# Performance work log

Measured on AMD Instinct MI355X. Metric: run time of the kernel, lower is better.

Reference implementation:

```python
import jax, jax.numpy as jnp
import numpy as np

B, S, D, H, HID = 2, 2048, 512, 8, 2048
DH = D // H
EPS = 1e-5


def _ln(x, g, b):
    mu = jnp.mean(x, axis=-1, keepdims=True)
    var = jnp.mean(jnp.square(x - mu), axis=-1, keepdims=True)
    return (x - mu) * jax.lax.rsqrt(var + EPS) * g + b


def setup_inputs() -> dict:
    key = jax.random.key(0)
    ks = jax.random.split(key, 12)
    s = 0.02
    return {
        "x": jax.random.normal(ks[0], (B, S, D), jnp.float32),
        "prev": jax.random.normal(ks[1], (B, H, S, S), jnp.float32),
        # weights stored as [in, out]
        "kqv_w": jax.random.normal(ks[2], (D, 3 * D), jnp.float32) * s,
        "kqv_b": jnp.zeros((3 * D,), jnp.float32),
        "out_w": jax.random.normal(ks[3], (D, D), jnp.float32) * s,
        "out_b": jnp.zeros((D,), jnp.float32),
        "fc1_w": jax.random.normal(ks[4], (D, HID), jnp.float32) * s,
        "fc1_b": jnp.zeros((HID,), jnp.float32),
        "fc2_w": jax.random.normal(ks[5], (HID, D), jnp.float32) * s,
        "fc2_b": jnp.zeros((D,), jnp.float32),
        "ln1_g": jnp.ones((D,), jnp.float32),
        "ln1_b": jnp.zeros((D,), jnp.float32),
        "ln2_g": jnp.ones((D,), jnp.float32),
        "ln2_b": jnp.zeros((D,), jnp.float32),
    }


def reference(x, prev, kqv_w, kqv_b, out_w, out_b, fc1_w, fc1_b, fc2_w, fc2_b,
              ln1_g, ln1_b, ln2_g, ln2_b):
    scale = 1.0 / np.sqrt(DH)
    kqv = x @ kqv_w + kqv_b                      # [B,S,3D]
    # torch.chunk order: key, query, value
    k, q, v = jnp.split(kqv, 3, axis=-1)
    k = k.reshape(B, S, H, DH)
    q = q.reshape(B, S, H, DH)
    v = v.reshape(B, S, H, DH)
    energy = scale * jnp.einsum('bqhd,bkhd->bhqk', q, k) + prev  # [B,H,S,S]
    attn = jax.nn.softmax(energy, axis=-1)
    ctx = jnp.einsum('bhqk,bkhd->bqhd', attn, v).reshape(B, S, D)
    attn_out = ctx @ out_w + out_b
    h = _ln(attn_out + x, ln1_g, ln1_b)          # post-norm 1
    ff = jax.nn.gelu(h @ fc1_w + fc1_b, approximate=False) @ fc2_w + fc2_b
    out = _ln(ff + h, ln2_g, ln2_b)              # post-norm 2
    return (out, energy)
```

## Files before the change

kernel.cpp:

```cpp
#include <hip/hip_runtime.h>
#include <math.h>

#define S_ 2048
#define D_ 512
#define H_ 8
#define DH_ 64
#define HID_ 2048
#define NT_ 4096
#define K3D_ 1536

typedef unsigned short u16;
typedef __bf16 bf16x8 __attribute__((ext_vector_type(8)));
typedef float f32x4 __attribute__((ext_vector_type(4)));

__device__ __forceinline__ float b2f(u16 u) {
  union { unsigned int i; float f; } v; v.i = ((unsigned int)u) << 16; return v.f;
}
__device__ __forceinline__ u16 f2b(float f) {
  union { float f; unsigned int i; } v; v.f = f;
  unsigned int u = v.i;
  u += 0x7fffu + ((u >> 16) & 1u);
  return (u16)(u >> 16);
}

__global__ __launch_bounds__(256) void cvt_kernel(
    const float* __restrict__ in, u16* __restrict__ out, int n8) {
  int i = blockIdx.x * 256 + threadIdx.x;
  if (i >= n8) return;
  size_t base = (size_t)i * 8;
  float4 a = *(const float4*)(in + base);
  float4 b = *(const float4*)(in + base + 4);
  u16 ov[8] = {f2b(a.x), f2b(a.y), f2b(a.z), f2b(a.w),
               f2b(b.x), f2b(b.y), f2b(b.z), f2b(b.w)};
  *(uint4*)(out + base) = *(uint4*)ov;
}

__global__ __launch_bounds__(256) void transpose_kernel(
    const float* __restrict__ in, u16* __restrict__ out, int R, int C) {
  int idx = blockIdx.x * 256 + threadIdx.x;
  if (idx >= R * C) return;
  int r = idx / C, c = idx % C;
  out[(size_t)c * R + r] = f2b(in[idx]);
}

__global__ __launch_bounds__(256) void vt_kernel(
    const u16* __restrict__ kqv, u16* __restrict__ vt) {
  int bh = blockIdx.y, b = bh >> 3, h = bh & 7;
  const u16* V = kqv + (size_t)b * S_ * K3D_ + 2 * D_ + h * DH_;
  u16* O = vt + (size_t)bh * DH_ * S_;
  int idx = blockIdx.x * 256 + threadIdx.x;
  int r = idx >> 6, c = idx & 63;
  O[(size_t)c * S_ + r] = V[(size_t)r * K3D_ + c];
}

__global__ __launch_bounds__(256) void gemm_bt(
    const u16* __restrict__ A, const u16* __restrict__ Bt,
    const float* __restrict__ bias, void* __restrict__ Cv,
    int K, int lda, int ldb, int ldc, int mode) {
  u16* Cb = (u16*)Cv;
  int tile_m = blockIdx.y * 64, tile_n = blockIdx.x * 64;

  __shared__ alignas(16) u16 As[64 * 40];
  __shared__ alignas(16) u16 Bs[64 * 40];

  int t = threadIdx.x;
  int w = t >> 6, lane = t & 63, quad = lane >> 4, l16 = lane & 15;
  int srow = t >> 2, schunk = (t & 3) * 8;

  f32x4 acc[4];
#pragma unroll
  for (int i = 0; i < 4; ++i) acc[i] = (f32x4){0.f, 0.f, 0.f, 0.f};

  for (int kb = 0; kb < K; kb += 32) {
    uint4 av = *(const uint4*)(A  + (size_t)(tile_m + srow) * lda + kb + schunk);
    uint4 bv = *(const uint4*)(Bt + (size_t)(tile_n + srow) * ldb + kb + schunk);
    __syncthreads();
    *(uint4*)(&As[srow * 40 + schunk]) = av;
    *(uint4*)(&Bs[srow * 40 + schunk]) = bv;
    __syncthreads();
    bf16x8 a = *(const bf16x8*)(&As[(w * 16 + l16) * 40 + quad * 8]);
#pragma unroll
    for (int nt = 0; nt < 4; ++nt) {
      bf16x8 b = *(const bf16x8*)(&Bs[(nt * 16 + l16) * 40 + quad * 8]);
      acc[nt] = __builtin_amdgcn_mfma_f32_16x16x32_bf16(a, b, acc[nt], 0, 0, 0);
    }
  }

#pragma unroll
  for (int nt = 0; nt < 4; ++nt) {
    int col = tile_n + nt * 16 + l16;
    float bcol = bias[col];
#pragma unroll
    for (int r = 0; r < 4; ++r) {
      int row = tile_m + w * 16 + quad * 4 + r;
      float v = acc[nt][r] + bcol;
      if (mode == 1) v = 0.5f * v * (1.f + erff(v * 0.70710678118654752f));
      Cb[(size_t)row * ldc + col] = f2b(v);
    }
  }
}

__global__ __launch_bounds__(256) void fused_attn(
    const u16* __restrict__ kqv, const u16* __restrict__ vt,
    const float* __restrict__ prev, float* __restrict__ energy,
    u16* __restrict__ ctx) {
  int bh = blockIdx.y, b = bh >> 3, h = bh & 7;
  int qbase = blockIdx.x * 64;

  const u16* Qp  = kqv + (size_t)b * S_ * K3D_ + D_ + h * DH_;
  const u16* Kp  = kqv + (size_t)b * S_ * K3D_ + h * DH_;
  const u16* Vtp = vt + (size_t)bh * DH_ * S_;
  const float* Pvp = prev + (size_t)bh * S_ * S_;
  float* Ep = energy + (size_t)bh * S_ * S_;

  int t = threadIdx.x;
  int w = t >> 6, lane = t & 63, quad = lane >> 4, l16 = lane & 15;

  __shared__ alignas(16) u16 KsB[2][64 * 72];
  __shared__ alignas(16) u16 VsB[2][64 * 72];
  __shared__ alignas(16) float Es[4][16 * 68];
  __shared__ alignas(16) u16 Pt[4][16 * 72];
  __shared__ float m_s[4][16];
  __shared__ float l_s[4][16];
  __shared__ float r_s[4][16];

  bf16x8 qf0, qf1;
  {
    const u16* qrow = Qp + (size_t)(qbase + w * 16 + l16) * K3D_;
    qf0 = *(const bf16x8*)(qrow + quad * 8);
    qf1 = *(const bf16x8*)(qrow + 32 + quad * 8);
  }

  if (lane < 16) { m_s[w][lane] = -1e30f; l_s[w][lane] = 0.f; }

  f32x4 oa[4];
#pragma unroll
  for (int i = 0; i < 4; ++i) oa[i] = (f32x4){0.f, 0.f, 0.f, 0.f};

  int c0 = t * 2, c1 = c0 + 1;
  int kr0 = c0 >> 3, ko0 = (c0 & 7) * 8;
  int kr1 = c1 >> 3, ko1 = (c1 & 7) * 8;

  {
    uint4 ka0 = *(const uint4*)(Kp + (size_t)kr0 * K3D_ + ko0);
    uint4 ka1 = *(const uint4*)(Kp + (size_t)kr1 * K3D_ + ko1);
    uint4 va0 = *(const uint4*)(Vtp + (size_t)kr0 * S_ + ko0);
    uint4 va1 = *(const uint4*)(Vtp + (size_t)kr1 * S_ + ko1);
    *(uint4*)(&KsB[0][kr0 * 72 + ko0]) = ka0;
    *(uint4*)(&KsB[0][kr1 * 72 + ko1]) = ka1;
    *(uint4*)(&VsB[0][kr0 * 72 + ko0]) = va0;
    *(uint4*)(&VsB[0][kr1 * 72 + ko1]) = va1;
  }
  __syncthreads();

  for (int it = 0; it < 32; ++it) {
    int cur = it & 1;
    int kb = it * 64;

    uint4 ka0, ka1, va0, va1;
    if (it < 31) {
      int kn = kb + 64;
      ka0 = *(const uint4*)(Kp + (size_t)(kn + kr0) * K3D_ + ko0);
      ka1 = *(const uint4*)(Kp + (size_t)(kn + kr1) * K3D_ + ko1);
      va0 = *(const uint4*)(Vtp + (size_t)kr0 * S_ + kn + ko0);
      va1 = *(const uint4*)(Vtp + (size_t)kr1 * S_ + kn + ko1);
    }

    const u16* Ks = KsB[cur];
    const u16* Vs = VsB[cur];

    f32x4 sa[4];
#pragma unroll
    for (int i = 0; i < 4; ++i) sa[i] = (f32x4){0.f, 0.f, 0.f, 0.f};
#pragma unroll
    for (int kc = 0; kc < 2; ++kc) {
      bf16x8 a = kc ? qf1 : qf0;
#pragma unroll
      for (int nt = 0; nt < 4; ++nt) {
        bf16x8 bk = *(const bf16x8*)(&Ks[(nt * 16 + l16) * 72 + kc * 32 + quad * 8]);
        sa[nt] = __builtin_amdgcn_mfma_f32_16x16x32_bf16(a, bk, sa[nt], 0, 0, 0);
      }
    }

#pragma unroll
    for (int nt = 0; nt < 4; ++nt)
#pragma unroll
      for (int r = 0; r < 4; ++r)
        Es[w][(quad * 4 + r) * 68 + nt * 16 + l16] = sa[nt][r] * 0.125f;
    asm volatile("" ::: "memory");

    float4 ek[4];
    float mt[4];
#pragma unroll
    for (int r4 = 0; r4 < 4; ++r4) {
      int row = r4 * 4 + quad;
      float4 e4 = *(const float4*)(&Es[w][row * 68 + l16 * 4]);
      size_t goff = (size_t)(qbase + w * 16 + row) * S_ + kb + l16 * 4;
      float4 p4 = *(const float4*)(Pvp + goff);
      e4.x += p4.x; e4.y += p4.y; e4.z += p4.z; e4.w += p4.w;
      *(float4*)(Ep + goff) = e4;
      ek[r4] = e4;
      mt[r4] = fmaxf(fmaxf(e4.x, e4.y), fmaxf(e4.z, e4.w));
    }
#pragma unroll
    for (int r4 = 0; r4 < 4; ++r4)
#pragma unroll
      for (int off = 1; off < 16; off <<= 1)
        mt[r4] = fmaxf(mt[r4], __shfl_xor(mt[r4], off, 16));
    if (l16 == 0) {
#pragma unroll
      for (int r4 = 0; r4 < 4; ++r4) {
        int row = r4 * 4 + quad;
        float mo = m_s[w][row];
        float mn = fmaxf(mo, mt[r4]);
        r_s[w][row] = __expf(mo - mn);
        m_s[w][row] = mn;
      }
    }
    asm volatile("" ::: "memory");

    float ls[4];
#pragma unroll
    for (int r4 = 0; r4 < 4; ++r4) {
      int row = r4 * 4 + quad;
      float mrow = m_s[w][row];
      float4 e4 = ek[r4];
      float p0 = __expf(e4.x - mrow), p1 = __expf(e4.y - mrow);
      float p2 = __expf(e4.z - mrow), p3 = __expf(e4.w - mrow);
      ls[r4] = (p0 + p1) + (p2 + p3);
      u16 pb[4] = {f2b(p0), f2b(p1), f2b(p2), f2b(p3)};
      *(uint2*)(&Pt[w][row * 72 + l16 * 4]) = *(uint2*)pb;
    }
#pragma unroll
    for (int r4 = 0; r4 < 4; ++r4)
#pragma unroll
      for (int off = 1; off < 16; off <<= 1)
        ls[r4] += __shfl_xor(ls[r4], off, 16);
    if (l16 == 0) {
#pragma unroll
      for (int r4 = 0; r4 < 4; ++r4) {
        int row = r4 * 4 + quad;
        l_s[w][row] = l_s[w][row] * r_s[w][row] + ls[r4];
      }
    }
#pragma unroll
    for (int rr = 0; rr < 4; ++rr) {
      float rf = r_s[w][quad * 4 + rr];
#pragma unroll
      for (int nt = 0; nt < 4; ++nt) oa[nt][rr] *= rf;
    }
    asm volatile("" ::: "memory");

#pragma unroll
    for (int kc = 0; kc < 2; ++kc) {
      bf16x8 a = *(const bf16x8*)(&Pt[w][l16 * 72 + kc * 32 + quad * 8]);
#pragma unroll
      for (int nt = 0; nt < 4; ++nt) {
        bf16x8 bv = *(const bf16x8*)(&Vs[(nt * 16 + l16) * 72 + kc * 32 + quad * 8]);
        oa[nt] = __builtin_amdgcn_mfma_f32_16x16x32_bf16(a, bv, oa[nt], 0, 0, 0);
      }
    }

    if (it < 31) {
      int nxt = cur ^ 1;
      *(uint4*)(&KsB[nxt][kr0 * 72 + ko0]) = ka0;
      *(uint4*)(&KsB[nxt][kr1 * 72 + ko1]) = ka1;
      *(uint4*)(&VsB[nxt][kr0 * 72 + ko0]) = va0;
      *(uint4*)(&VsB[nxt][kr1 * 72 + ko1]) = va1;
      __syncthreads();
    }
  }

  asm volatile("" ::: "memory");
  float il[4];
#pragma unroll
  for (int rr = 0; rr < 4; ++rr) il[rr] = 1.f / l_s[w][quad * 4 + rr];
#pragma unroll
  for (int nt = 0; nt < 4; ++nt) {
    int col = h * DH_ + nt * 16 + l16;
#pragma unroll
    for (int rr = 0; rr < 4; ++rr) {
      size_t row = (size_t)b * S_ + qbase + w * 16 + quad * 4 + rr;
      ctx[row * D_ + col] = f2b(oa[nt][rr] * il[rr]);
    }
  }
}

__global__ __launch_bounds__(256) void ln_kernel(
    const u16* __restrict__ a, const void* __restrict__ rsrc,
    const float* __restrict__ g, const float* __restrict__ be,
    void* __restrict__ o, int r_f32, int o_f32) {
  int row = blockIdx.x * 4 + (threadIdx.x >> 6);
  int lane = threadIdx.x & 63;
  size_t base = (size_t)row * D_ + lane * 8;
  uint4 av = *(const uint4*)(a + base);
  const u16* ap = (const u16*)&av;
  float rv[8];
  if (r_f32) {
    float4 r0 = *(const float4*)((const float*)rsrc + base);
    float4 r1 = *(const float4*)((const float*)rsrc + base + 4);
    rv[0] = r0.x; rv[1] = r0.y; rv[2] = r0.z; rv[3] = r0.w;
    rv[4] = r1.x; rv[5] = r1.y; rv[6] = r1.z; rv[7] = r1.w;
  } else {
    uint4 rr = *(const uint4*)((const u16*)rsrc + base);
    const u16* rp = (const u16*)&rr;
#pragma unroll
    for (int j = 0; j < 8; ++j) rv[j] = b2f(rp[j]);
  }
  float tv[8], s = 0.f, sq = 0.f;
#pragma unroll
  for (int j = 0; j < 8; ++j) {
    float xx = b2f(ap[j]) + rv[j];
    tv[j] = xx; s += xx; sq += xx * xx;
  }
#pragma unroll
  for (int off = 32; off; off >>= 1) {
    s  += __shfl_xor(s, off);
    sq += __shfl_xor(sq, off);
  }
  float mu  = s * (1.f / 512.f);
  float var = fmaxf(sq * (1.f / 512.f) - mu * mu, 0.f);
  float wv  = rsqrtf(var + 1e-5f);
  float4 g0 = *(const float4*)(g + lane * 8);
  float4 g1 = *(const float4*)(g + lane * 8 + 4);
  float4 b0 = *(const float4*)(be + lane * 8);
  float4 b1 = *(const float4*)(be + lane * 8 + 4);
  float gv[8] = {g0.x, g0.y, g0.z, g0.w, g1.x, g1.y, g1.z, g1.w};
  float bv[8] = {b0.x, b0.y, b0.z, b0.w, b1.x, b1.y, b1.z, b1.w};
  if (o_f32) {
    float ov[8];
#pragma unroll
    for (int j = 0; j < 8; ++j) ov[j] = (tv[j] - mu) * wv * gv[j] + bv[j];
    *(float4*)((float*)o + base)     = *(float4*)(ov);
    *(float4*)((float*)o + base + 4) = *(float4*)(ov + 4);
  } else {
    u16 ov[8];
#pragma unroll
    for (int j = 0; j < 8; ++j) ov[j] = f2b((tv[j] - mu) * wv * gv[j] + bv[j]);
    *(uint4*)((u16*)o + base) = *(uint4*)ov;
  }
}

extern "C" void kernel_launch(void* const* d_in, const int* in_sizes, int n_in,
                              void* d_out, int out_size, void* d_ws, size_t ws_size,
                              hipStream_t stream) {
  const float* x     = (const float*)d_in[0];
  const float* prev  = (const float*)d_in[1];
  const float* kqv_w = (const float*)d_in[2];
  const float* kqv_b = (const float*)d_in[3];
  const float* out_w = (const float*)d_in[4];
  const float* out_b = (const float*)d_in[5];
  const float* fc1_w = (const float*)d_in[6];
  const float* fc1_b = (const float*)d_in[7];
  const float* fc2_w = (const float*)d_in[8];
  const float* fc2_b = (const float*)d_in[9];
  const float* ln1_g = (const float*)d_in[10];
  const float* ln1_b = (const float*)d_in[11];
  const float* ln2_g = (const float*)d_in[12];
  const float* ln2_b = (const float*)d_in[13];

  float* outp   = (float*)d_out;
  float* energy = outp + (size_t)NT_ * D_;

  u16* ws = (u16*)d_ws;
  u16* R0 = ws;
  u16* R2 = R0 + (size_t)8388608;
  u16* R3 = R2 + (size_t)2097152;
  u16* R4 = R3 + (size_t)2097152;
  u16* WA = R4 + (size_t)2097152;

  u16* kqv    = R0;
  u16* vt     = R0 + (size_t)6291456;
  u16* attn   = R0;
  u16* ff     = R0;
  u16* ctx    = R2;  u16* f2     = R2;
  u16* hbuf   = R3;
  u16* xb     = R4;
  u16* fc1_wt = R4;  u16* fc2_wt = R4 + (size_t)1048576;
  u16* kqv_wt = WA;  u16* out_wt = WA;

  cvt_kernel<<<(NT_ * D_ / 8 + 255) / 256, 256, 0, stream>>>(x, xb, NT_ * D_ / 8);
  transpose_kernel<<<(D_ * K3D_ + 255) / 256, 256, 0, stream>>>(kqv_w, kqv_wt, D_, K3D_);

  gemm_bt<<<dim3(K3D_ / 64, NT_ / 64, 1), 256, 0, stream>>>(
      xb, kqv_wt, kqv_b, kqv, D_, D_, D_, K3D_, 0);

  transpose_kernel<<<(D_ * HID_ + 255) / 256, 256, 0, stream>>>(fc1_w, fc1_wt, D_, HID_);
  transpose_kernel<<<(HID_ * D_ + 255) / 256, 256, 0, stream>>>(fc2_w, fc2_wt, HID_, D_);
  transpose_kernel<<<(D_ * D_ + 255) / 256, 256, 0, stream>>>(out_w, out_wt, D_, D_);

  vt_kernel<<<dim3((S_ * DH_) / 256, 16), 256, 0, stream>>>(kqv, vt);

  fused_attn<<<dim3(S_ / 64, 16), 256, 0, stream>>>(kqv, vt, prev, energy, ctx);

  gemm_bt<<<dim3(D_ / 64, NT_ / 64, 1), 256, 0, stream>>>(
      ctx, out_wt, out_b, attn, D_, D_, D_, D_, 0);

  ln_kernel<<<NT_ / 4, 256, 0, stream>>>(attn, x, ln1_g, ln1_b, hbuf, 1, 0);

  gemm_bt<<<dim3(HID_ / 64, NT_ / 64, 1), 256, 0, stream>>>(
      hbuf, fc1_wt, fc1_b, ff, D_, D_, D_, HID_, 1);

  gemm_bt<<<dim3(D_ / 64, NT_ / 64, 1), 256, 0, stream>>>(
      ff, fc2_wt, fc2_b, f2, HID_, HID_, HID_, D_, 0);

  ln_kernel<<<NT_ / 4, 256, 0, stream>>>(f2, hbuf, ln2_g, ln2_b, outp, 0, 1);
}
```

Before: 661.3 us.

## Replace GEMM with larger-tile kernel using direct global-to-LDS loads

Replaces the 64x64 GEMM with a templated kernel using 128xBN tiles, a 2x2 wave layout and multiple MFMAs per K step for more register reuse. Tiles are loaded with global_load_lds straight into shared memory, skipping the trip through registers. The LDS padding is removed, which may add bank conflicts, and larger tiles mean fewer blocks for the narrow N=512 GEMMs.

After: 678.7 us. 1.03x slower.

```diff
diff --git a/kernel.cpp b/kernel.cpp
--- a/kernel.cpp
+++ b/kernel.cpp
@@ -12,6 +12,9 @@
 typedef unsigned short u16;
 typedef __bf16 bf16x8 __attribute__((ext_vector_type(8)));
 typedef float f32x4 __attribute__((ext_vector_type(4)));
+
+typedef const __attribute__((address_space(1))) unsigned int* gas_p;
+typedef __attribute__((address_space(3))) unsigned int* las_p;
 
 __device__ __forceinline__ float b2f(u16 u) {
   union { unsigned int i; float f; } v; v.i = ((unsigned int)u) << 16; return v.f;
@@ -53,49 +56,77 @@
   O[(size_t)c * S_ + r] = V[(size_t)r * K3D_ + c];
 }
 
-__global__ __launch_bounds__(256) void gemm_bt(
+template<int BN>
+__global__ __launch_bounds__(256) void gemm_glds(
     const u16* __restrict__ A, const u16* __restrict__ Bt,
-    const float* __restrict__ bias, void* __restrict__ Cv,
-    int K, int lda, int ldb, int ldc, int mode) {
-  u16* Cb = (u16*)Cv;
-  int tile_m = blockIdx.y * 64, tile_n = blockIdx.x * 64;
-
-  __shared__ alignas(16) u16 As[64 * 40];
-  __shared__ alignas(16) u16 Bs[64 * 40];
+    const float* __restrict__ bias, u16* __restrict__ C,
+    int K, int lda, int ldb, int ldc, int gelu) {
+  constexpr int BM = 128;
+  constexpr int NF = BN / 32;
+  constexpr int A_LOADS = BM / 64;
+  constexpr int B_LOADS = BN / 64;
+
+  __shared__ alignas(16) u16 As[BM * 32];
+  __shared__ alignas(16) u16 Bs[BN * 32];
 
   int t = threadIdx.x;
   int w = t >> 6, lane = t & 63, quad = lane >> 4, l16 = lane & 15;
-  int srow = t >> 2, schunk = (t & 3) * 8;
-
-  f32x4 acc[4];
-#pragma unroll
-  for (int i = 0; i < 4; ++i) acc[i] = (f32x4){0.f, 0.f, 0.f, 0.f};
+  int wr = w >> 1, wc = w & 1;
+  int tile_m = blockIdx.y * BM, tile_n = blockIdx.x * BN;
+
+  int srow = lane >> 2, schunk = (lane & 3) * 8;
+
+  f32x4 acc[4][NF];
+#pragma unroll
+  for (int i = 0; i < 4; ++i)
+#pragma unroll
+    for (int n = 0; n < NF; ++n) acc[i][n] = (f32x4){0.f, 0.f, 0.f, 0.f};
 
   for (int kb = 0; kb < K; kb += 32) {
-    uint4 av = *(const uint4*)(A  + (size_t)(tile_m + srow) * lda + kb + schunk);
-    uint4 bv = *(const uint4*)(Bt + (size_t)(tile_n + srow) * ldb + kb + schunk);
     __syncthreads();
-    *(uint4*)(&As[srow * 40 + schunk]) = av;
-    *(uint4*)(&Bs[srow * 40 + schunk]) = bv;
+#pragma unroll
+    for (int j = 0; j < A_LOADS; ++j) {
+      int jj = w * A_LOADS + j;
+      const u16* g = A + (size_t)(tile_m + jj * 16 + srow) * lda + kb + schunk;
+      __builtin_amdgcn_global_load_lds((gas_p)(const void*)g,
+                                       (las_p)(void*)(As + jj * 512), 16, 0, 0);
+    }
+#pragma unroll
+    for (int j = 0; j < B_LOADS; ++j) {
+      int jj = w * B_LOADS + j;
+      const u16* g = Bt + (size_t)(tile_n + jj * 16 + srow) * ldb + kb + schunk;
+      __builtin_amdgcn_global_load_lds((gas_p)(const void*)g,
+                                       (las_p)(void*)(Bs + jj * 512), 16, 0, 0);
+    }
     __syncthreads();
-    bf16x8 a = *(const bf16x8*)(&As[(w * 16 + l16) * 40 + quad * 8]);
-#pragma unroll
-    for (int nt = 0; nt < 4; ++nt) {
-      bf16x8 b = *(const bf16x8*)(&Bs[(nt * 16 + l16) * 40 + quad * 8]);
-      acc[nt] = __builtin_amdgcn_mfma_f32_16x16x32_bf16(a, b, acc[nt], 0, 0, 0);
-    }
-  }
-
-#pragma unroll
-  for (int nt = 0; nt < 4; ++nt) {
-    int col = tile_n + nt * 16 + l16;
+
+    bf16x8 af[4], bfr[NF];
+#pragma unroll
+    for (int i = 0; i < 4; ++i)
+      af[i] = *(const bf16x8*)(&As[(wr * 64 + i * 16 + l16) * 32 + quad * 8]);
+#pragma unroll
+    for (int n = 0; n < NF; ++n)
+      bfr[n] = *(const bf16x8*)(&Bs[(wc * (BN / 2) + n * 16 + l16) * 32 + quad * 8]);
+#pragma unroll
+    for (int i = 0; i < 4; ++i)
+#pragma unroll
+      for (int n = 0; n < NF; ++n)
+        acc[i][n] = __builtin_amdgcn_mfma_f32_16x16x32_bf16(af[i], bfr[n], acc[i][n], 0, 0, 0);
+  }
+
+#pragma unroll
+  for (int n = 0; n < NF; ++n) {
+    int col = tile_n + wc * (BN / 2) + n * 16 + l16;
     float bcol = bias[col];
 #pragma unroll
-    for (int r = 0; r < 4; ++r) {
-      int row = tile_m + w * 16 + quad * 4 + r;
-      float v = acc[nt][r] + bcol;
-      if (mode == 1) v = 0.5f * v * (1.f + erff(v * 0.70710678118654752f));
-      Cb[(size_t)row * ldc + col] = f2b(v);
+    for (int i = 0; i < 4; ++i) {
+#pragma unroll
+      for (int r = 0; r < 4; ++r) {
+        int row = tile_m + wr * 64 + i * 16 + quad * 4 + r;
+        float v = acc[i][n][r] + bcol;
+        if (gelu) v = 0.5f * v * (1.f + erff(v * 0.70710678118654752f));
+        C[(size_t)row * ldc + col] = f2b(v);
+      }
     }
   }
 }
@@ -382,7 +413,7 @@
   cvt_kernel<<<(NT_ * D_ / 8 + 255) / 256, 256, 0, stream>>>(x, xb, NT_ * D_ / 8);
   transpose_kernel<<<(D_ * K3D_ + 255) / 256, 256, 0, stream>>>(kqv_w, kqv_wt, D_, K3D_);
 
-  gemm_bt<<<dim3(K3D_ / 64, NT_ / 64, 1), 256, 0, stream>>>(
+  gemm_glds<128><<<dim3(K3D_ / 128, NT_ / 128, 1), 256, 0, stream>>>(
       xb, kqv_wt, kqv_b, kqv, D_, D_, D_, K3D_, 0);
 
   transpose_kernel<<<(D_ * HID_ + 255) / 256, 256, 0, stream>>>(fc1_w, fc1_wt, D_, HID_);
@@ -393,15 +424,15 @@
 
   fused_attn<<<dim3(S_ / 64, 16), 256, 0, stream>>>(kqv, vt, prev, energy, ctx);
 
-  gemm_bt<<<dim3(D_ / 64, NT_ / 64, 1), 256, 0, stream>>>(
+  gemm_glds<64><<<dim3(D_ / 64, NT_ / 128, 1), 256, 0, stream>>>(
       ctx, out_wt, out_b, attn, D_, D_, D_, D_, 0);
 
   ln_kernel<<<NT_ / 4, 256, 0, stream>>>(attn, x, ln1_g, ln1_b, hbuf, 1, 0);
 
-  gemm_bt<<<dim3(HID_ / 64, NT_ / 64, 1), 256, 0, stream>>>(
+  gemm_glds<128><<<dim3(HID_ / 128, NT_ / 128, 1), 256, 0, stream>>>(
       hbuf, fc1_wt, fc1_b, ff, D_, D_, D_, HID_, 1);
 
-  gemm_bt<<<dim3(D_ / 64, NT_ / 64, 1), 256, 0, stream>>>(
+  gemm_glds<64><<<dim3(D_ / 64, NT_ / 128, 1), 256, 0, stream>>>(
       ff, fc2_wt, fc2_b, f2, HID_, HID_, HID_, D_, 0);
 
   ln_kernel<<<NT_ / 4, 256, 0, stream>>>(f2, hbuf, ln2_g, ln2_b, outp, 0, 1);
```
